# Kernel tuning notes

Hardware: AMD Instinct MI355X
Metric: run time of the kernel (lower is better)

## Reference

```python
import jax, jax.numpy as jnp
import numpy as np

N_NODES = 100000
N_EDGES = 1600000
IN_CH = 64
HID_CH = 128


def setup_inputs() -> dict:
    key = jax.random.key(0)
    k1, k2, k3, k4, k5 = jax.random.split(key, 5)
    x = jax.random.normal(k1, (N_NODES, IN_CH), dtype=jnp.float32)
    edge_index = jax.random.randint(k2, (2, N_EDGES), 0, N_NODES, dtype=jnp.int64)
    emb_weight = jax.random.normal(k3, (N_NODES, IN_CH), dtype=jnp.float32) * 0.1
    lin_l_w = jax.random.normal(k4, (IN_CH, HID_CH), dtype=jnp.float32) * (1.0 / np.sqrt(IN_CH))
    lin_l_b = jnp.zeros((HID_CH,), dtype=jnp.float32)
    lin_r_w = jax.random.normal(k5, (IN_CH, HID_CH), dtype=jnp.float32) * (1.0 / np.sqrt(IN_CH))
    return {"x": x, "edge_index": edge_index, "emb_weight": emb_weight,
            "lin_l_w": lin_l_w, "lin_l_b": lin_l_b, "lin_r_w": lin_r_w}


def reference(x, edge_index, emb_weight, lin_l_w, lin_l_b, lin_r_w):
    # forward ignores x and uses the embedding table directly
    h = emb_weight  # F.dropout in eval mode is the identity
    dst = edge_index[0]  # row of adj_t (aggregation target)
    src = edge_index[1]  # col of adj_t (neighbor source)
    # mean aggregation of neighbor features: [E, IN] gather + segment sum
    msgs = h[src]
    agg = jax.ops.segment_sum(msgs, dst, num_segments=N_NODES)
    deg = jax.ops.segment_sum(jnp.ones((N_EDGES,), h.dtype), dst, num_segments=N_NODES)
    mean = agg / jnp.maximum(deg, 1.0)[:, None]
    # SAGEConv: lin_l(aggregated neighbors) + lin_r(self) + bias
    out = mean @ lin_l_w + h @ lin_r_w + lin_l_b
    return out
```

## Files before the change

### kernel.cpp

```cpp
#include <hip/hip_runtime.h>

#define N_NODES 100000
#define N_EDGES 1600000
#define IN_CH 64
#define HID_CH 128

#define BIN_SZ 256
#define BIN_BITS 8
#define NBINS ((N_NODES + BIN_SZ - 1) / BIN_SZ)
#define BIN_CAP 4864
#define SEPB 8192
#define STAGE_BLOCKS ((N_EDGES + SEPB - 1) / SEPB)
#define CVT_BLOCKS 768
#define BIN_CACHE 8192

typedef __attribute__((ext_vector_type(8))) short bf16x8;
typedef __attribute__((ext_vector_type(4))) float f32x4;

static __device__ __forceinline__ unsigned short f2bf(float f) {
    union { float f; unsigned int u; } v; v.f = f;
    const unsigned int u = v.u;
    return (unsigned short)((u + 0x7FFFu + ((u >> 16) & 1u)) >> 16);
}

#define UNPACK_ADD(A, V) do {                                         \
    union { unsigned int u; float f; } lo_, hi_;                      \
    _Pragma("unroll")                                                 \
    for (int j_ = 0; j_ < 4; ++j_) {                                  \
        const unsigned int w_ = (&(V).x)[j_];                         \
        lo_.u = w_ << 16;         A[2 * j_] += lo_.f;                 \
        hi_.u = w_ & 0xFFFF0000u; A[2 * j_ + 1] += hi_.f;             \
    } } while (0)

__global__ __launch_bounds__(256) void sage_stage(
    const int* __restrict__ ei, int* __restrict__ bin_cursor,
    int* __restrict__ stage)
{
    __shared__ int s_cnt[NBINS];
    __shared__ int s_base[NBINS];
    const int t = threadIdx.x;
    for (int i = t; i < NBINS; i += 256) s_cnt[i] = 0;
    __syncthreads();
    const int e0 = blockIdx.x * SEPB;
#pragma unroll
    for (int k = 0; k < 32; ++k) {
        const int e = e0 + k * 256 + t;
        if (e < N_EDGES) atomicAdd(&s_cnt[ei[e] >> BIN_BITS], 1);
    }
    __syncthreads();
    for (int i = t; i < NBINS; i += 256) {
        const int c = s_cnt[i];
        s_base[i] = (c > 0) ? (i * BIN_CAP + atomicAdd(&bin_cursor[i], c)) : 0;
        s_cnt[i] = 0;
    }
    __syncthreads();
#pragma unroll
    for (int k = 0; k < 32; ++k) {
        const int e = e0 + k * 256 + t;
        if (e < N_EDGES) {
            const int dst = ei[e];
            const int src = ei[N_EDGES + e];
            const int bin = dst >> BIN_BITS;
            const int p = s_base[bin] + atomicAdd(&s_cnt[bin], 1);
            if (p < (bin + 1) * BIN_CAP)
                stage[p] = ((dst & (BIN_SZ - 1)) << 17) | src;
        }
    }
}

__global__ __launch_bounds__(256) void sage_bucket2(
    const int* __restrict__ stage, const int* __restrict__ bin_cursor,
    const float* __restrict__ Wl, const float* __restrict__ Wr,
    const float* __restrict__ h, unsigned short* __restrict__ hb,
    unsigned short* __restrict__ Bt, int* __restrict__ node_cnt,
    int* __restrict__ node_start, int* __restrict__ bucket)
{
    const int b = blockIdx.x;
    const int t = threadIdx.x;

    if (b >= NBINS) {
        const int n4 = N_NODES * IN_CH / 4;
        for (int i = (b - NBINS) * 256 + t; i < n4; i += CVT_BLOCKS * 256) {
            const float4 v = reinterpret_cast<const float4*>(h)[i];
            ushort4 o;
            o.x = f2bf(v.x); o.y = f2bf(v.y); o.z = f2bf(v.z); o.w = f2bf(v.w);
            reinterpret_cast<ushort4*>(hb)[i] = o;
        }
        return;
    }

    __shared__ int s_cnt[BIN_SZ];
    __shared__ int s_off[BIN_SZ];
    __shared__ int s_cur[BIN_SZ];
    __shared__ int s_edges[BIN_CACHE];
    {
        const int wi = b * 256 + t;
        if (wi < HID_CH * HID_CH) {
            const int n = wi >> 7, k = wi & 127;
            const float v = (k < 64) ? Wl[k * HID_CH + n] : Wr[(k - 64) * HID_CH + n];
            Bt[wi] = f2bf(v);
        }
    }
    s_cnt[t] = 0; s_cur[t] = 0;
    __syncthreads();
    const int start = b * BIN_CAP;
    int len = bin_cursor[b];
    len = (len > BIN_CAP) ? BIN_CAP : len;
    const bool cached = (len <= BIN_CACHE);
    if (cached) {
        for (int i = t; i < len; i += 256) {
            const int p = stage[start + i];
            s_edges[i] = p;
            atomicAdd(&s_cnt[p >> 17], 1);
        }
    } else {
        for (int i = t; i < len; i += 256)
            atomicAdd(&s_cnt[stage[start + i] >> 17], 1);
    }
    __syncthreads();
    const int v = s_cnt[t];
    s_off[t] = v;
    __syncthreads();
    for (int off = 1; off < 256; off <<= 1) {
        const int a = (t >= off) ? s_off[t - off] : 0;
        __syncthreads();
        s_off[t] += a;
        __syncthreads();
    }
    const int excl = s_off[t] - v;
    s_off[t] = excl;
    __syncthreads();
    const int node = (b << BIN_BITS) + t;
    if (node < N_NODES) {
        node_cnt[node] = v;
        node_start[node] = start + excl;
    }
    if (cached) {
        for (int i = t; i < len; i += 256) {
            const int p = s_edges[i];
            const int l = p >> 17;
            bucket[start + s_off[l] + atomicAdd(&s_cur[l], 1)] = p & 0x1FFFF;
        }
    } else {
        for (int i = t; i < len; i += 256) {
            const int p = stage[start + i];
            const int l = p >> 17;
            bucket[start + s_off[l] + atomicAdd(&s_cur[l], 1)] = p & 0x1FFFF;
        }
    }
}

__global__ __launch_bounds__(256) void sage_gmfma(
    const int* __restrict__ node_cnt, const int* __restrict__ node_start,
    const int* __restrict__ bucket, const unsigned short* __restrict__ hb,
    const unsigned short* __restrict__ Bt, const float* __restrict__ bias,
    float* __restrict__ out)
{
    __shared__ unsigned short s_mean[16][72];
    const int t = threadIdx.x;
    const int w = t >> 6;
    const int lane = t & 63;
    const int sub = lane >> 3;
    const int c8 = lane & 7;
    const int node0 = blockIdx.x * 16;

    int d_[4], st_[4];
#pragma unroll
    for (int nn = 0; nn < 4; ++nn) {
        const int node = node0 + w * 4 + nn;
        d_[nn] = node_cnt[node];
        st_[nn] = node_start[node];
    }
    int maxd = d_[0];
#pragma unroll
    for (int nn = 1; nn < 4; ++nn) maxd = (d_[nn] > maxd) ? d_[nn] : maxd;

    float a0[8] = {0.f,0.f,0.f,0.f,0.f,0.f,0.f,0.f};
    float a1[8] = {0.f,0.f,0.f,0.f,0.f,0.f,0.f,0.f};
    float a2[8] = {0.f,0.f,0.f,0.f,0.f,0.f,0.f,0.f};
    float a3[8] = {0.f,0.f,0.f,0.f,0.f,0.f,0.f,0.f};

    for (int g = 0; g < maxd; g += 8) {
        const int e = g + sub;
        int s0 = -1, s1 = -1, s2 = -1, s3 = -1;
        if (e < d_[0]) s0 = bucket[st_[0] + e];
        if (e < d_[1]) s1 = bucket[st_[1] + e];
        if (e < d_[2]) s2 = bucket[st_[2] + e];
        if (e < d_[3]) s3 = bucket[st_[3] + e];
        if (s0 >= 0) {
            const uint4 v = *reinterpret_cast<const uint4*>(hb + (size_t)s0 * IN_CH + c8 * 8);
            UNPACK_ADD(a0, v);
        }
        if (s1 >= 0) {
            const uint4 v = *reinterpret_cast<const uint4*>(hb + (size_t)s1 * IN_CH + c8 * 8);
            UNPACK_ADD(a1, v);
        }
        if (s2 >= 0) {
            const uint4 v = *reinterpret_cast<const uint4*>(hb + (size_t)s2 * IN_CH + c8 * 8);
            UNPACK_ADD(a2, v);
        }
        if (s3 >= 0) {
            const uint4 v = *reinterpret_cast<const uint4*>(hb + (size_t)s3 * IN_CH + c8 * 8);
            UNPACK_ADD(a3, v);
        }
    }

#define REDUCE_STORE(A, NN) do {                                        \
    _Pragma("unroll")                                                   \
    for (int j = 0; j < 8; ++j) {                                       \
        A[j] += __shfl_xor(A[j], 8);                                    \
        A[j] += __shfl_xor(A[j], 16);                                   \
        A[j] += __shfl_xor(A[j], 32);                                   \
    }                                                                   \
    if (sub == 0) {                                                     \
        const float inv = 1.0f / (float)((d_[NN] > 1) ? d_[NN] : 1);    \
        uint4 o;                                                        \
        _Pragma("unroll")                                               \
        for (int j = 0; j < 4; ++j) {                                   \
            const unsigned int l = f2bf(A[2 * j] * inv);                \
            const unsigned int hh = f2bf(A[2 * j + 1] * inv);           \
            (&o.x)[j] = l | (hh << 16);                                 \
        }                                                               \
        *reinterpret_cast<uint4*>(&s_mean[w * 4 + NN][c8 * 8]) = o;     \
    } } while (0)

    REDUCE_STORE(a0, 0);
    REDUCE_STORE(a1, 1);
    REDUCE_STORE(a2, 2);
    REDUCE_STORE(a3, 3);
#undef REDUCE_STORE

    __syncthreads();

    const int lrow = lane & 15;
    const int lk8 = (lane >> 4) * 8;

    bf16x8 a[4];
    a[0] = *reinterpret_cast<const bf16x8*>(&s_mean[lrow][lk8]);
    a[1] = *reinterpret_cast<const bf16x8*>(&s_mean[lrow][32 + lk8]);
    {
        const unsigned short* ah = hb + (size_t)(node0 + lrow) * IN_CH;
        a[2] = *reinterpret_cast<const bf16x8*>(ah + lk8);
        a[3] = *reinterpret_cast<const bf16x8*>(ah + 32 + lk8);
    }

#pragma unroll
    for (int c = 0; c < 2; ++c) {
        const int ct = 2 * w + c;
        f32x4 acc2 = (f32x4){0.f, 0.f, 0.f, 0.f};
#pragma unroll
        for (int kk = 0; kk < 4; ++kk) {
            const bf16x8 b = *reinterpret_cast<const bf16x8*>(
                Bt + (size_t)(ct * 16 + lrow) * 128 + kk * 32 + lk8);
            acc2 = __builtin_amdgcn_mfma_f32_16x16x32_bf16(a[kk], b, acc2, 0, 0, 0);
        }
        const int ch = ct * 16 + lrow;
        const float bv = bias[ch];
#pragma unroll
        for (int r = 0; r < 4; ++r) {
            const int node = node0 + (lane >> 4) * 4 + r;
            out[(size_t)node * HID_CH + ch] = acc2[r] + bv;
        }
    }
}


__global__ __launch_bounds__(256) void sage_scatter(
    const int* __restrict__ ei, const float* __restrict__ h,
    float* __restrict__ agg, float* __restrict__ deg)
{
    const int gtid = blockIdx.x * blockDim.x + threadIdx.x;
    const int edge = gtid >> 6;
    const int lane = threadIdx.x & 63;
    if (edge >= N_EDGES) return;
    const int dst = ei[edge];
    const int src = ei[N_EDGES + edge];
    atomicAdd(&agg[(size_t)dst * IN_CH + lane], h[(size_t)src * IN_CH + lane]);
    if (lane == 0) atomicAdd(&deg[dst], 1.0f);
}

__global__ __launch_bounds__(128) void sage_node(
    const float* __restrict__ h, const float* __restrict__ agg,
    const float* __restrict__ deg, const float* __restrict__ Wl,
    const float* __restrict__ bias, const float* __restrict__ Wr,
    float* __restrict__ out)
{
    const int t = threadIdx.x;
    float wl[IN_CH], wr[IN_CH];
#pragma unroll
    for (int k = 0; k < IN_CH; ++k) {
        wl[k] = Wl[k * HID_CH + t];
        wr[k] = Wr[k * HID_CH + t];
    }
    const float b = bias[t];
    __shared__ float s_mean[IN_CH];
    __shared__ float s_h[IN_CH];
    for (int n = blockIdx.x; n < N_NODES; n += gridDim.x) {
        __syncthreads();
        if (t < IN_CH) {
            const float inv = 1.0f / fmaxf(deg[n], 1.0f);
            s_mean[t] = agg[(size_t)n * IN_CH + t] * inv;
            s_h[t] = h[(size_t)n * IN_CH + t];
        }
        __syncthreads();
        float acc = b;
#pragma unroll
        for (int k = 0; k < IN_CH; ++k) {
            acc = fmaf(s_mean[k], wl[k], acc);
            acc = fmaf(s_h[k], wr[k], acc);
        }
        out[(size_t)n * HID_CH + t] = acc;
    }
}

extern "C" void kernel_launch(void* const* d_in, const int* in_sizes, int n_in,
                              void* d_out, int out_size, void* d_ws, size_t ws_size,
                              hipStream_t stream) {
    const int* ei = (const int*)d_in[1];
    const float* h = (const float*)d_in[2];
    const float* Wl = (const float*)d_in[3];
    const float* b = (const float*)d_in[4];
    const float* Wr = (const float*)d_in[5];
    float* out = (float*)d_out;

    const size_t need = 7600000ull * 4ull;

    if (ws_size >= need) {
        int* wsi = (int*)d_ws;
        int* node_cnt = wsi;
        int* node_start = wsi + 100000;
        int* bin_cursor = wsi + 200000;
        unsigned short* Bt = (unsigned short*)(wsi + 200400);
        int* bucket = wsi + 400000;
        int* stage = wsi + 2400000;
        unsigned short* hb = (unsigned short*)(wsi + 4400000);

        hipMemsetAsync(bin_cursor, 0, NBINS * sizeof(int), stream);

        sage_stage<<<STAGE_BLOCKS, 256, 0, stream>>>(ei, bin_cursor, stage);
        sage_bucket2<<<NBINS + CVT_BLOCKS, 256, 0, stream>>>(
            stage, bin_cursor, Wl, Wr, h, hb, Bt, node_cnt, node_start, bucket);
        sage_gmfma<<<N_NODES / 16, 256, 0, stream>>>(node_cnt, node_start, bucket, hb, Bt, b, out);
    } else {
        float* agg = (float*)d_ws;
        float* deg = agg + (size_t)N_NODES * IN_CH;
        hipMemsetAsync(d_ws, 0, ((size_t)N_NODES * IN_CH + N_NODES) * sizeof(float), stream);
        sage_scatter<<<(int)(((long long)N_EDGES * 64 + 255) / 256), 256, 0, stream>>>(ei, h, agg, deg);
        sage_node<<<4096, 128, 0, stream>>>(h, agg, deg, Wl, b, Wr, out);
    }
}
```

Measured before the change: 130.8 us.

## Prefetch next neighbor indices in gather loop and halve stage block size

The aggregation loop now loads the next group of bucket indices before consuming the current ones, software-pipelining the index load against the dependent feature gather. Out-of-range loads are clamped to index 0 and masked, so loads are unconditional. Separately, the staging kernel processes 4096 edges per block instead of 8192, doubling the block count for more parallelism at the cost of more global atomics on bin cursors.

Result: no change. 128.7 us (-1.6%).

```diff
diff --git a/kernel.cpp b/kernel.cpp
--- a/kernel.cpp
+++ b/kernel.cpp
@@ -9,7 +9,7 @@
 #define BIN_BITS 8
 #define NBINS ((N_NODES + BIN_SZ - 1) / BIN_SZ)
 #define BIN_CAP 4864
-#define SEPB 8192
+#define SEPB 4096
 #define STAGE_BLOCKS ((N_EDGES + SEPB - 1) / SEPB)
 #define CVT_BLOCKS 768
 #define BIN_CACHE 8192
@@ -43,7 +43,7 @@
     __syncthreads();
     const int e0 = blockIdx.x * SEPB;
 #pragma unroll
-    for (int k = 0; k < 32; ++k) {
+    for (int k = 0; k < SEPB / 256; ++k) {
         const int e = e0 + k * 256 + t;
         if (e < N_EDGES) atomicAdd(&s_cnt[ei[e] >> BIN_BITS], 1);
     }
@@ -55,7 +55,7 @@
     }
     __syncthreads();
 #pragma unroll
-    for (int k = 0; k < 32; ++k) {
+    for (int k = 0; k < SEPB / 256; ++k) {
         const int e = e0 + k * 256 + t;
         if (e < N_EDGES) {
             const int dst = ei[e];
@@ -180,13 +180,29 @@
     float a2[8] = {0.f,0.f,0.f,0.f,0.f,0.f,0.f,0.f};
     float a3[8] = {0.f,0.f,0.f,0.f,0.f,0.f,0.f,0.f};
 
+    int s0, s1, s2, s3;
+    {
+        const int e = sub;
+        int i0 = bucket[st_[0] + ((e < d_[0]) ? e : 0)];
+        int i1 = bucket[st_[1] + ((e < d_[1]) ? e : 0)];
+        int i2 = bucket[st_[2] + ((e < d_[2]) ? e : 0)];
+        int i3 = bucket[st_[3] + ((e < d_[3]) ? e : 0)];
+        s0 = (e < d_[0]) ? i0 : -1;
+        s1 = (e < d_[1]) ? i1 : -1;
+        s2 = (e < d_[2]) ? i2 : -1;
+        s3 = (e < d_[3]) ? i3 : -1;
+    }
+
     for (int g = 0; g < maxd; g += 8) {
-        const int e = g + sub;
-        int s0 = -1, s1 = -1, s2 = -1, s3 = -1;
-        if (e < d_[0]) s0 = bucket[st_[0] + e];
-        if (e < d_[1]) s1 = bucket[st_[1] + e];
-        if (e < d_[2]) s2 = bucket[st_[2] + e];
-        if (e < d_[3]) s3 = bucket[st_[3] + e];
+        const int en = g + 8 + sub;
+        int n0 = bucket[st_[0] + ((en < d_[0]) ? en : 0)];
+        int n1 = bucket[st_[1] + ((en < d_[1]) ? en : 0)];
+        int n2 = bucket[st_[2] + ((en < d_[2]) ? en : 0)];
+        int n3 = bucket[st_[3] + ((en < d_[3]) ? en : 0)];
+        n0 = (en < d_[0]) ? n0 : -1;
+        n1 = (en < d_[1]) ? n1 : -1;
+        n2 = (en < d_[2]) ? n2 : -1;
+        n3 = (en < d_[3]) ? n3 : -1;
         if (s0 >= 0) {
             const uint4 v = *reinterpret_cast<const uint4*>(hb + (size_t)s0 * IN_CH + c8 * 8);
             UNPACK_ADD(a0, v);
@@ -203,6 +219,7 @@
             const uint4 v = *reinterpret_cast<const uint4*>(hb + (size_t)s3 * IN_CH + c8 * 8);
             UNPACK_ADD(a3, v);
         }
+        s0 = n0; s1 = n1; s2 = n2; s3 = n3;
     }
 
 #define REDUCE_STORE(A, NN) do {                                        \
```
